# Optimization experiments

Measured on AMD Instinct MI355X. Metric: run time of the kernel, lower is better.

## Reference

```python
import jax, jax.numpy as jnp
import numpy as np

B, T, C, H = 4, 2048, 1024, 16
NEG = -1e9  # masked-fill value (finite to keep grads clean)


def setup_inputs() -> dict:
    key = jax.random.key(0)
    ks = jax.random.split(key, 5)
    s = 1.0 / np.sqrt(C)  # keep logits O(1) like trained linear layers
    return {
        "x": jax.random.normal(ks[0], (B, T, C), dtype=jnp.float32),
        "wq": jax.random.normal(ks[1], (C, C), dtype=jnp.float32) * s,
        "bq": jnp.zeros((C,), dtype=jnp.float32),
        "wk": jax.random.normal(ks[2], (C, C), dtype=jnp.float32) * s,
        "bk": jnp.zeros((C,), dtype=jnp.float32),
        "wv": jax.random.normal(ks[3], (C, C), dtype=jnp.float32) * s,
        "bv": jnp.zeros((C,), dtype=jnp.float32),
        "wo": jax.random.normal(ks[4], (C, C), dtype=jnp.float32) * s,
        "bo": jnp.zeros((C,), dtype=jnp.float32),
    }


def _split_heads(y):
    # [B,T,C] -> [B,H,T,hd]
    b, t, c = y.shape
    return y.reshape(b, t, H, c // H).transpose(0, 2, 1, 3)


def reference(x, wq, bq, wk, bk, wv, bv, wo, bo):
    b, t, c = x.shape
    scale = (c // H) ** (-0.5)
    q = _split_heads(x @ wq.T + bq)  # [B,H,T,hd]
    k = _split_heads(x @ wk.T + bk)
    v = _split_heads(x @ wv.T + bv)
    att = jnp.einsum("bhqd,bhkd->bhqk", q, k) * scale  # [B,H,T,T]
    causal = jnp.tril(jnp.ones((t, t), dtype=bool))
    att = jnp.where(causal[None, None], att, NEG)
    att = jax.nn.softmax(att, axis=-1)  # dropout is identity in eval mode
    y = jnp.einsum("bhqk,bhkd->bhqd", att, v)
    y = y.transpose(0, 2, 1, 3).reshape(b, t, c)
    return y @ wo.T + bo
```

## Files before the change

kernel.cpp:

```cpp
#include <hip/hip_runtime.h>


#define B_ 4
#define T_ 2048
#define C_ 1024
#define H_ 16
#define M_ 8192

typedef unsigned short u16;
typedef __bf16 bf16x8 __attribute__((ext_vector_type(8)));
typedef float f32x4 __attribute__((ext_vector_type(4)));

static __device__ __forceinline__ u16 f2bf(float f) {
  unsigned int u = __float_as_uint(f);
  u += 0x7fffu + ((u >> 16) & 1u);
  return (u16)(u >> 16);
}

static __device__ __forceinline__ void async16(const void* g, void* l) {
  __builtin_amdgcn_global_load_lds(
      (const __attribute__((address_space(1))) unsigned int*)g,
      (__attribute__((address_space(3))) unsigned int*)l, 16, 0, 0);
}

#if __has_builtin(__builtin_amdgcn_exp2f)
#define EXP2F(x) __builtin_amdgcn_exp2f(x)
#else
#define EXP2F(x) exp2f(x)
#endif

static __device__ __forceinline__ f32x4 mfma32(bf16x8 a, bf16x8 b, f32x4 c) {
  return __builtin_amdgcn_mfma_f32_16x16x32_bf16(a, b, c, 0, 0, 0);
}

static __device__ __forceinline__ unsigned int cvtpk(float lo, float hi) {
  unsigned int r;
  asm("v_cvt_pk_bf16_f32 %0, %1, %2" : "=v"(r) : "v"(lo), "v"(hi));
  return r;
}

#define FENCE() asm volatile("" ::: "memory")

__global__ __launch_bounds__(256) void cvt_all(const float* __restrict__ x,
                                               const float* __restrict__ w0,
                                               const float* __restrict__ w1,
                                               const float* __restrict__ w2,
                                               const float* __restrict__ w3,
                                               u16* __restrict__ xb,
                                               u16* __restrict__ wb,
                                               float s0) {
  const int NX = M_ * C_ / 4, NW = C_ * C_ / 4;
  int i = blockIdx.x * 256 + threadIdx.x;
  const float* src;
  u16* dst;
  int idx;
  float s = 1.f;
  if (i < NX) {
    src = x; dst = xb; idx = i;
  } else {
    int j = i - NX;
    int w = j / NW;
    idx = j - w * NW;
    src = (w == 0) ? w0 : (w == 1) ? w1 : (w == 2) ? w2 : w3;
    dst = wb + (size_t)w * C_ * C_;
    if (w == 0) s = s0;
  }
  float4 f = ((const float4*)src)[idx];
  ushort4 o;
  o.x = f2bf(f.x * s); o.y = f2bf(f.y * s); o.z = f2bf(f.z * s); o.w = f2bf(f.w * s);
  ((ushort4*)dst)[idx] = o;
}

__global__ __launch_bounds__(512, 1) void gemm_qkv(const u16* __restrict__ A,
                                                   const u16* __restrict__ W,
                                                   const float* __restrict__ bq,
                                                   const float* __restrict__ bk,
                                                   const float* __restrict__ bv,
                                                   float qscale,
                                                   u16* __restrict__ outqk,
                                                   u16* __restrict__ vtb) {
  __shared__ __align__(16) union {
    u16 buf[3][24576];
    u16 Cu[256 * 136];
    u16 Ct[128 * 272];
  } sm;
  const int tid = threadIdx.x, lane = tid & 63, wave = tid >> 6;
  const int quad = lane >> 4, l16 = lane & 15;
  const int wm = wave >> 1, wn = wave & 1;
  const int bid = blockIdx.x;
  const int xcd = bid & 7, idx = bid >> 3;
  const int cq = idx >> 2;
  const int row0 = (xcd * 4 + (idx & 3)) * 256;
  const int sel = cq >> 3, colw = cq & 7;
  const int col0 = colw * 128;
  const u16* Bt = W + (size_t)sel * C_ * C_;
  const float* bias = sel == 0 ? bq : (sel == 1 ? bk : bv);
  const float bscale = sel == 0 ? qscale : 1.f;

  const u16* aptr[4];
  const u16* bptr[2];
#pragma unroll
  for (int it = 0; it < 4; it++) {
    int c = it * 512 + tid, r = c >> 3, g = (c & 7) ^ (r & 7);
    aptr[it] = A + (size_t)(row0 + r) * C_ + g * 8;
  }
#pragma unroll
  for (int it = 0; it < 2; it++) {
    int c = it * 512 + tid, r = c >> 3, g = (c & 7) ^ (r & 7);
    bptr[it] = Bt + (size_t)(col0 + r) * C_ + g * 8;
  }

  auto STAGE = [&](int t, int pp) {
    const int k0 = t * 64;
    u16* lA = sm.buf[pp];
    u16* lB = sm.buf[pp] + 16384;
#pragma unroll
    for (int it = 0; it < 4; it++)
      async16(aptr[it] + k0, lA + (size_t)(it * 512 + wave * 64) * 8);
#pragma unroll
    for (int it = 0; it < 2; it++)
      async16(bptr[it] + k0, lB + (size_t)(it * 512 + wave * 64) * 8);
  };

  f32x4 zero = {0.f, 0.f, 0.f, 0.f};
  f32x4 acc[4][4];
#pragma unroll
  for (int i = 0; i < 4; i++)
#pragma unroll
    for (int j = 0; j < 4; j++) acc[i][j] = zero;

  STAGE(0, 0);
  STAGE(1, 1);

  int p = 0, p2 = 2;
#pragma unroll 1
  for (int u = 0; u < 16; ++u) {
    FENCE();
    __builtin_amdgcn_s_barrier();
    FENCE();
    if (u < 14) STAGE(u + 2, p2);
    if (u < 14) {
      asm volatile("s_waitcnt vmcnt(12)" ::: "memory");
    } else if (u < 15) {
      asm volatile("s_waitcnt vmcnt(6)" ::: "memory");
    } else {
      asm volatile("s_waitcnt vmcnt(0)" ::: "memory");
    }
    FENCE();
    __builtin_amdgcn_s_barrier();
    FENCE();

    const u16* As = sm.buf[p];
    const u16* Bs = sm.buf[p] + 16384;
    bf16x8 bfr[4][2];
#pragma unroll
    for (int j = 0; j < 4; j++) {
      int rn = wn * 64 + 16 * j + l16;
#pragma unroll
      for (int kk = 0; kk < 2; kk++)
        bfr[j][kk] =
            *(const bf16x8*)(Bs + rn * 64 + (((kk * 4 + quad) ^ (rn & 7)) * 8));
    }
    {
      bf16x8 a2[2][2];
#pragma unroll
      for (int i = 0; i < 2; i++) {
        int rm = wm * 64 + 16 * i + l16;
#pragma unroll
        for (int kk = 0; kk < 2; kk++)
          a2[i][kk] =
              *(const bf16x8*)(As + rm * 64 + (((kk * 4 + quad) ^ (rm & 7)) * 8));
      }
      __builtin_amdgcn_s_setprio(1);
#pragma unroll
      for (int i = 0; i < 2; i++)
#pragma unroll
        for (int j = 0; j < 4; j++) {
          acc[i][j] = mfma32(a2[i][0], bfr[j][0], acc[i][j]);
          acc[i][j] = mfma32(a2[i][1], bfr[j][1], acc[i][j]);
        }
      __builtin_amdgcn_s_setprio(0);
    }
    FENCE();
    __builtin_amdgcn_s_barrier();
    FENCE();
    {
      bf16x8 a2[2][2];
#pragma unroll
      for (int i = 0; i < 2; i++) {
        int rm = wm * 64 + 16 * (i + 2) + l16;
#pragma unroll
        for (int kk = 0; kk < 2; kk++)
          a2[i][kk] =
              *(const bf16x8*)(As + rm * 64 + (((kk * 4 + quad) ^ (rm & 7)) * 8));
      }
      __builtin_amdgcn_s_setprio(1);
#pragma unroll
      for (int i = 0; i < 2; i++)
#pragma unroll
        for (int j = 0; j < 4; j++) {
          acc[i + 2][j] = mfma32(a2[i][0], bfr[j][0], acc[i + 2][j]);
          acc[i + 2][j] = mfma32(a2[i][1], bfr[j][1], acc[i + 2][j]);
        }
      __builtin_amdgcn_s_setprio(0);
    }
    asm volatile("s_waitcnt lgkmcnt(0)" ::: "memory");
    p = (p == 2) ? 0 : p + 1;
    p2 = (p2 == 2) ? 0 : p2 + 1;
  }
  __syncthreads();

  float bj[4];
#pragma unroll
  for (int j = 0; j < 4; j++) bj[j] = bias[col0 + wn * 64 + 16 * j + l16] * bscale;

  if (sel == 2) {
#pragma unroll
    for (int i = 0; i < 4; i++)
#pragma unroll
      for (int j = 0; j < 4; j++) {
        int lc = wn * 64 + 16 * j + l16;
        int rt = wm * 64 + 16 * i + quad * 4;
        union { u16 s[4]; uint2 u; } w;
#pragma unroll
        for (int r = 0; r < 4; r++) w.s[r] = f2bf(acc[i][j][r] + bj[j]);
        *(uint2*)(sm.Ct + (size_t)lc * 272 + rt) = w.u;
      }
    __syncthreads();
    const int bb = row0 >> 11, t0 = row0 & 2047;
#pragma unroll
    for (int c2 = 0; c2 < 8; c2++) {
      int c = c2 * 512 + tid;
      int nr = c >> 5, ch = c & 31;
      bf16x8 v = *(const bf16x8*)(sm.Ct + (size_t)nr * 272 + ch * 8);
      int gn = col0 + nr, d = gn & 63, hh = gn >> 6;
      *(bf16x8*)(vtb + ((size_t)((bb * 16 + hh) * 64 + d)) * T_ + t0 + ch * 8) = v;
    }
  } else {
#pragma unroll
    for (int i = 0; i < 4; i++)
#pragma unroll
      for (int j = 0; j < 4; j++) {
        int lc = wn * 64 + 16 * j + l16;
        int rt = wm * 64 + 16 * i + quad * 4;
#pragma unroll
        for (int r = 0; r < 4; r++)
          sm.Cu[(size_t)(rt + r) * 136 + lc] = f2bf(acc[i][j][r] + bj[j]);
      }
    __syncthreads();
    u16* dst = outqk + (size_t)sel * M_ * C_;
#pragma unroll
    for (int c2 = 0; c2 < 8; c2++) {
      int c = c2 * 512 + tid;
      int rw = c >> 4, ch = c & 15;
      bf16x8 v = *(const bf16x8*)(sm.Cu + (size_t)rw * 136 + ch * 8);
      *(bf16x8*)(dst + (size_t)(row0 + rw) * C_ + col0 + ch * 8) = v;
    }
  }
}

__global__ __launch_bounds__(512, 1) void gemm_o(const u16* __restrict__ A,
                                                 const u16* __restrict__ Bt,
                                                 const float* __restrict__ bias,
                                                 float* __restrict__ outf) {
  __shared__ __align__(16) union {
    u16 buf[3][24576];
    float Cf[256 * 132];
  } sm;
  const int tid = threadIdx.x, lane = tid & 63, wave = tid >> 6;
  const int quad = lane >> 4, l16 = lane & 15;
  const int wm = wave >> 1, wn = wave & 1;
  const int bid = blockIdx.x;
  const int xcd = bid & 7, idx = bid >> 3;
  const int row0 = (xcd * 4 + (idx & 3)) * 256;
  const int col0 = (idx >> 2) * 128;

  const u16* aptr[4];
  const u16* bptr[2];
#pragma unroll
  for (int it = 0; it < 4; it++) {
    int c = it * 512 + tid, r = c >> 3, g = (c & 7) ^ (r & 7);
    aptr[it] = A + (size_t)(row0 + r) * C_ + g * 8;
  }
#pragma unroll
  for (int it = 0; it < 2; it++) {
    int c = it * 512 + tid, r = c >> 3, g = (c & 7) ^ (r & 7);
    bptr[it] = Bt + (size_t)(col0 + r) * C_ + g * 8;
  }

  auto STAGE = [&](int t, int pp) {
    const int k0 = t * 64;
    u16* lA = sm.buf[pp];
    u16* lB = sm.buf[pp] + 16384;
#pragma unroll
    for (int it = 0; it < 4; it++)
      async16(aptr[it] + k0, lA + (size_t)(it * 512 + wave * 64) * 8);
#pragma unroll
    for (int it = 0; it < 2; it++)
      async16(bptr[it] + k0, lB + (size_t)(it * 512 + wave * 64) * 8);
  };

  f32x4 zero = {0.f, 0.f, 0.f, 0.f};
  f32x4 acc[4][4];
#pragma unroll
  for (int i = 0; i < 4; i++)
#pragma unroll
    for (int j = 0; j < 4; j++) acc[i][j] = zero;

  STAGE(0, 0);
  STAGE(1, 1);

  int p = 0, p2 = 2;
#pragma unroll 1
  for (int u = 0; u < 16; ++u) {
    FENCE();
    __builtin_amdgcn_s_barrier();
    FENCE();
    if (u < 14) STAGE(u + 2, p2);
    if (u < 14) {
      asm volatile("s_waitcnt vmcnt(12)" ::: "memory");
    } else if (u < 15) {
      asm volatile("s_waitcnt vmcnt(6)" ::: "memory");
    } else {
      asm volatile("s_waitcnt vmcnt(0)" ::: "memory");
    }
    FENCE();
    __builtin_amdgcn_s_barrier();
    FENCE();

    const u16* As = sm.buf[p];
    const u16* Bs = sm.buf[p] + 16384;
    bf16x8 bfr[4][2];
#pragma unroll
    for (int j = 0; j < 4; j++) {
      int rn = wn * 64 + 16 * j + l16;
#pragma unroll
      for (int kk = 0; kk < 2; kk++)
        bfr[j][kk] =
            *(const bf16x8*)(Bs + rn * 64 + (((kk * 4 + quad) ^ (rn & 7)) * 8));
    }
    {
      bf16x8 a2[2][2];
#pragma unroll
      for (int i = 0; i < 2; i++) {
        int rm = wm * 64 + 16 * i + l16;
#pragma unroll
        for (int kk = 0; kk < 2; kk++)
          a2[i][kk] =
              *(const bf16x8*)(As + rm * 64 + (((kk * 4 + quad) ^ (rm & 7)) * 8));
      }
      __builtin_amdgcn_s_setprio(1);
#pragma unroll
      for (int i = 0; i < 2; i++)
#pragma unroll
        for (int j = 0; j < 4; j++) {
          acc[i][j] = mfma32(a2[i][0], bfr[j][0], acc[i][j]);
          acc[i][j] = mfma32(a2[i][1], bfr[j][1], acc[i][j]);
        }
      __builtin_amdgcn_s_setprio(0);
    }
    FENCE();
    __builtin_amdgcn_s_barrier();
    FENCE();
    {
      bf16x8 a2[2][2];
#pragma unroll
      for (int i = 0; i < 2; i++) {
        int rm = wm * 64 + 16 * (i + 2) + l16;
#pragma unroll
        for (int kk = 0; kk < 2; kk++)
          a2[i][kk] =
              *(const bf16x8*)(As + rm * 64 + (((kk * 4 + quad) ^ (rm & 7)) * 8));
      }
      __builtin_amdgcn_s_setprio(1);
#pragma unroll
      for (int i = 0; i < 2; i++)
#pragma unroll
        for (int j = 0; j < 4; j++) {
          acc[i + 2][j] = mfma32(a2[i][0], bfr[j][0], acc[i + 2][j]);
          acc[i + 2][j] = mfma32(a2[i][1], bfr[j][1], acc[i + 2][j]);
        }
      __builtin_amdgcn_s_setprio(0);
    }
    asm volatile("s_waitcnt lgkmcnt(0)" ::: "memory");
    p = (p == 2) ? 0 : p + 1;
    p2 = (p2 == 2) ? 0 : p2 + 1;
  }
  __syncthreads();

  float bj[4];
#pragma unroll
  for (int j = 0; j < 4; j++) bj[j] = bias[col0 + wn * 64 + 16 * j + l16];

#pragma unroll
  for (int i = 0; i < 4; i++)
#pragma unroll
    for (int j = 0; j < 4; j++) {
      int lc = wn * 64 + 16 * j + l16;
      int rt = wm * 64 + 16 * i + quad * 4;
#pragma unroll
      for (int r = 0; r < 4; r++)
        sm.Cf[(size_t)(rt + r) * 132 + lc] = acc[i][j][r] + bj[j];
    }
  __syncthreads();
#pragma unroll
  for (int c2 = 0; c2 < 16; c2++) {
    int c = c2 * 512 + tid;
    int rw = c >> 5, c4 = c & 31;
    float4 v = *(const float4*)(sm.Cf + (size_t)rw * 132 + c4 * 4);
    *(float4*)(outf + (size_t)(row0 + rw) * C_ + col0 + c4 * 4) = v;
  }
}

__global__ __launch_bounds__(256) void attn(const u16* __restrict__ q,
                                            const u16* __restrict__ k,
                                            const u16* __restrict__ vt,
                                            u16* __restrict__ y) {
  __shared__ __align__(16) u16 Ksm[128 * 64];
  __shared__ __align__(16) u16 Vsm[2][64 * 64];
  const int tid = threadIdx.x, lane = tid & 63, wave = tid >> 6;
  const int quad = lane >> 4, l16 = lane & 15;
  static const int qperm[16] = {15, 14, 11, 10, 12, 13, 8, 9, 3, 2, 7, 6, 0, 1, 4, 5};
  const int bh = blockIdx.x;
  const int qt = qperm[blockIdx.y];
  const int b = bh >> 4, h = bh & 15;

  const int S0 = ((lane & 15) + ((lane >> 4) & 1) * 32) * 4;
  const int S1 = S0 + 64;
  const bool hi32 = (lane & 32) != 0;

  bf16x8 qf[2][2];
#pragma unroll
  for (int m = 0; m < 2; m++) {
    const u16* qp =
        q + (size_t)(b * T_ + qt * 128 + wave * 32 + m * 16 + l16) * C_ + h * 64;
#pragma unroll
    for (int ks = 0; ks < 2; ks++)
      qf[m][ks] = *(const bf16x8*)(qp + ks * 32 + quad * 8);
  }

  f32x4 zero = {0.f, 0.f, 0.f, 0.f};
  f32x4 o[2][4];
  float lps[2] = {0.f, 0.f};
#pragma unroll
  for (int m = 0; m < 2; m++)
#pragma unroll
    for (int dt = 0; dt < 4; dt++) o[m][dt] = zero;

  const u16* kp[4];
  const u16* vp[4];
#pragma unroll
  for (int i = 0; i < 4; i++) {
    int c = i * 256 + tid;
    int r = c >> 3, lc = (c & 7) ^ (r & 7);
    kp[i] = k + (size_t)(b * T_ + r) * C_ + h * 64 + lc * 8;
  }
#pragma unroll
  for (int s = 0; s < 2; s++)
#pragma unroll
    for (int i = 0; i < 2; i++) {
      int c = i * 256 + tid;
      int r = c >> 3, lc = (c & 7) ^ (r & 7);
      vp[s * 2 + i] = vt + (size_t)(bh * 64 + r) * T_ + 64 * s + lc * 8;
    }

  const int qrow = wave * 32 + l16;

#pragma unroll 1
  for (int jt = 0; jt <= qt; ++jt) {
#pragma unroll
    for (int i = 0; i < 4; i++) {
      async16(kp[i], Ksm + (size_t)(i * 256 + wave * 64) * 8);
      kp[i] += (size_t)128 * C_;
    }
#pragma unroll
    for (int s = 0; s < 2; s++)
#pragma unroll
      for (int i = 0; i < 2; i++) {
        async16(vp[s * 2 + i], Vsm[s] + (size_t)(i * 256 + wave * 64) * 8);
        vp[s * 2 + i] += 128;
      }
    __syncthreads();

    const bool diag = (jt == qt);
#pragma unroll
    for (int hh = 0; hh < 2; ++hh) {
      if (diag && (2 * wave + 2 - 4 * hh) <= 0) continue;
      unsigned int pk[2][4][2];
#pragma unroll
      for (int n = 0; n < 4; ++n) {
        int rk = hh * 64 + n * 16 + l16;
        bf16x8 kf0 = *(const bf16x8*)(Ksm + rk * 64 + ((quad ^ (rk & 7)) * 8));
        bf16x8 kf1 = *(const bf16x8*)(Ksm + rk * 64 + (((4 + quad) ^ (rk & 7)) * 8));
#pragma unroll
        for (int m = 0; m < 2; ++m) {
          int nlim = diag ? (2 * wave + m + 1 - 4 * hh) : 4;
          float e[4];
          if (n < nlim) {
            f32x4 s = mfma32(kf0, qf[m][0], zero);
            s = mfma32(kf1, qf[m][1], s);
#pragma unroll
            for (int r = 0; r < 4; r++) e[r] = EXP2F(s[r]);
            if (diag) {
              int rmax = qrow + m * 16 - hh * 64 - n * 16 - quad * 4;
#pragma unroll
              for (int r = 0; r < 4; r++)
                if (r > rmax) e[r] = 0.f;
            }
            lps[m] += (e[0] + e[1]) + (e[2] + e[3]);
          } else {
#pragma unroll
            for (int r = 0; r < 4; r++) e[r] = 0.f;
          }
          pk[m][n][0] = cvtpk(e[0], e[1]);
          pk[m][n][1] = cvtpk(e[2], e[3]);
        }
      }
      bf16x8 pa[2][2];
#pragma unroll
      for (int m = 0; m < 2; ++m)
#pragma unroll
        for (int ks = 0; ks < 2; ++ks) {
          union { unsigned int u[4]; bf16x8 v; } uu;
#pragma unroll
          for (int c = 0; c < 2; ++c) {
            int x = (int)pk[m][2 * ks][c];
            int yv = (int)pk[m][2 * ks + 1][c];
            int bx0 = __builtin_amdgcn_ds_bpermute(S0, x);
            int by0 = __builtin_amdgcn_ds_bpermute(S0, yv);
            int bx1 = __builtin_amdgcn_ds_bpermute(S1, x);
            int by1 = __builtin_amdgcn_ds_bpermute(S1, yv);
            uu.u[c] = (unsigned int)(hi32 ? by0 : bx0);
            uu.u[2 + c] = (unsigned int)(hi32 ? by1 : bx1);
          }
          pa[m][ks] = uu.v;
        }
#pragma unroll
      for (int dt = 0; dt < 4; ++dt) {
        int rv = dt * 16 + l16;
        bf16x8 vf0 = *(const bf16x8*)(Vsm[hh] + rv * 64 + ((quad ^ (rv & 7)) * 8));
        bf16x8 vf1 = *(const bf16x8*)(Vsm[hh] + rv * 64 + (((4 + quad) ^ (rv & 7)) * 8));
#pragma unroll
        for (int m = 0; m < 2; m++) {
          o[m][dt] = mfma32(pa[m][0], vf0, o[m][dt]);
          o[m][dt] = mfma32(pa[m][1], vf1, o[m][dt]);
        }
      }
    }
    __syncthreads();
  }

  float linv[2];
#pragma unroll
  for (int m = 0; m < 2; m++) {
    float v = lps[m];
    v += __shfl_xor(v, 16);
    v += __shfl_xor(v, 32);
    linv[m] = 1.f / v;
  }

#pragma unroll
  for (int m = 0; m < 2; m++)
#pragma unroll
    for (int r = 0; r < 4; r++) {
      float il = __shfl(linv[m], quad * 4 + r);
      int grow = b * T_ + qt * 128 + wave * 32 + m * 16 + quad * 4 + r;
#pragma unroll
      for (int dt = 0; dt < 4; dt++)
        y[(size_t)grow * C_ + h * 64 + dt * 16 + l16] = f2bf(o[m][dt][r] * il);
    }
}

extern "C" void kernel_launch(void* const* d_in, const int* in_sizes, int n_in,
                              void* d_out, int out_size, void* d_ws, size_t ws_size,
                              hipStream_t stream) {
  const float* x  = (const float*)d_in[0];
  const float* wq = (const float*)d_in[1];
  const float* bq = (const float*)d_in[2];
  const float* wk = (const float*)d_in[3];
  const float* bk = (const float*)d_in[4];
  const float* wv = (const float*)d_in[5];
  const float* bv = (const float*)d_in[6];
  const float* wo = (const float*)d_in[7];
  const float* bo = (const float*)d_in[8];
  float* out = (float*)d_out;

  const float QSCALE = 0.125f * 1.4426950408889634f;

  u16* xb  = (u16*)d_ws;
  u16* wqb = xb  + (size_t)M_ * C_;
  u16* wob = wqb + 3 * (size_t)C_ * C_;
  u16* qb  = wob + (size_t)C_ * C_;
  u16* kb  = qb  + (size_t)M_ * C_;
  u16* vtb = kb  + (size_t)M_ * C_;
  u16* yb  = xb;

  const int NCVT = (M_ * C_ + 4 * C_ * C_) / 4 / 256;
  cvt_all<<<NCVT, 256, 0, stream>>>(x, wq, wk, wv, wo, xb, wqb, QSCALE);

  gemm_qkv<<<768, 512, 0, stream>>>(xb, wqb, bq, bk, bv, QSCALE, qb, vtb);

  attn<<<dim3(B_ * H_, 16), 256, 0, stream>>>(qb, kb, vtb, yb);

  gemm_o<<<256, 512, 0, stream>>>(yb, wob, bo, out);
}
```

Before: 251.5 us.

## Pair complementary causal query tiles per block and register-prefetch K/V tiles

Each attention block now handles query tile qtA and its mirror 15-qtA, so the causal work per block is even and each K/V tile loaded serves both tiles. The asynchronous global-to-LDS loads are replaced by register prefetching of the next K/V tile, which is written into LDS between two barriers. The grid drops to 512 blocks and register use rises, with two accumulator sets and the prefetch registers, which can lower occupancy.

```diff
diff --git a/kernel.cpp b/kernel.cpp
--- a/kernel.cpp
+++ b/kernel.cpp
@@ -420,32 +420,36 @@
   __shared__ __align__(16) u16 Vsm[2][64 * 64];
   const int tid = threadIdx.x, lane = tid & 63, wave = tid >> 6;
   const int quad = lane >> 4, l16 = lane & 15;
-  static const int qperm[16] = {15, 14, 11, 10, 12, 13, 8, 9, 3, 2, 7, 6, 0, 1, 4, 5};
   const int bh = blockIdx.x;
-  const int qt = qperm[blockIdx.y];
+  const int qtA = blockIdx.y;
+  const int qtB = 15 - qtA;
   const int b = bh >> 4, h = bh & 15;
 
   const int S0 = ((lane & 15) + ((lane >> 4) & 1) * 32) * 4;
   const int S1 = S0 + 64;
   const bool hi32 = (lane & 32) != 0;
 
-  bf16x8 qf[2][2];
+  bf16x8 qfA[2][2], qfB[2][2];
 #pragma unroll
   for (int m = 0; m < 2; m++) {
-    const u16* qp =
-        q + (size_t)(b * T_ + qt * 128 + wave * 32 + m * 16 + l16) * C_ + h * 64;
-#pragma unroll
-    for (int ks = 0; ks < 2; ks++)
-      qf[m][ks] = *(const bf16x8*)(qp + ks * 32 + quad * 8);
+    const u16* qpA =
+        q + (size_t)(b * T_ + qtA * 128 + wave * 32 + m * 16 + l16) * C_ + h * 64;
+    const u16* qpB =
+        q + (size_t)(b * T_ + qtB * 128 + wave * 32 + m * 16 + l16) * C_ + h * 64;
+#pragma unroll
+    for (int ks = 0; ks < 2; ks++) {
+      qfA[m][ks] = *(const bf16x8*)(qpA + ks * 32 + quad * 8);
+      qfB[m][ks] = *(const bf16x8*)(qpB + ks * 32 + quad * 8);
+    }
   }
 
   f32x4 zero = {0.f, 0.f, 0.f, 0.f};
-  f32x4 o[2][4];
-  float lps[2] = {0.f, 0.f};
+  f32x4 oA[2][4], oB[2][4];
+  float lpsA[2] = {0.f, 0.f}, lpsB[2] = {0.f, 0.f};
 #pragma unroll
   for (int m = 0; m < 2; m++)
 #pragma unroll
-    for (int dt = 0; dt < 4; dt++) o[m][dt] = zero;
+    for (int dt = 0; dt < 4; dt++) { oA[m][dt] = zero; oB[m][dt] = zero; }
 
   const u16* kp[4];
   const u16* vp[4];
@@ -464,25 +468,22 @@
       vp[s * 2 + i] = vt + (size_t)(bh * 64 + r) * T_ + 64 * s + lc * 8;
     }
 
+  uint4 kreg[4], vreg[4];
+  auto loadKV = [&](int jt) {
+    const size_t koff = (size_t)jt * 128 * C_;
+    const int voff = jt * 128;
+#pragma unroll
+    for (int i = 0; i < 4; i++)
+      kreg[i] = *(const uint4*)(kp[i] + koff);
+#pragma unroll
+    for (int i = 0; i < 4; i++)
+      vreg[i] = *(const uint4*)(vp[i] + voff);
+  };
+
   const int qrow = wave * 32 + l16;
 
-#pragma unroll 1
-  for (int jt = 0; jt <= qt; ++jt) {
-#pragma unroll
-    for (int i = 0; i < 4; i++) {
-      async16(kp[i], Ksm + (size_t)(i * 256 + wave * 64) * 8);
-      kp[i] += (size_t)128 * C_;
-    }
-#pragma unroll
-    for (int s = 0; s < 2; s++)
-#pragma unroll
-      for (int i = 0; i < 2; i++) {
-        async16(vp[s * 2 + i], Vsm[s] + (size_t)(i * 256 + wave * 64) * 8);
-        vp[s * 2 + i] += 128;
-      }
-    __syncthreads();
-
-    const bool diag = (jt == qt);
+  auto tileCompute = [&](const bf16x8 (&qf)[2][2], f32x4 (&o)[2][4],
+                         float (&lps)[2], const bool diag) {
 #pragma unroll
     for (int hh = 0; hh < 2; ++hh) {
       if (diag && (2 * wave + 2 - 4 * hh) <= 0) continue;
@@ -547,27 +548,60 @@
         }
       }
     }
-    __syncthreads();
-  }
-
-  float linv[2];
+  };
+
+  loadKV(0);
+
+#pragma unroll 1
+  for (int jt = 0; jt <= qtB; ++jt) {
+    FENCE();
+    __builtin_amdgcn_s_barrier();
+    FENCE();
+#pragma unroll
+    for (int i = 0; i < 4; i++)
+      *(uint4*)(Ksm + (size_t)(i * 256 + tid) * 8) = kreg[i];
+#pragma unroll
+    for (int s = 0; s < 2; s++)
+#pragma unroll
+      for (int i = 0; i < 2; i++)
+        *(uint4*)(Vsm[s] + (size_t)(i * 256 + tid) * 8) = vreg[s * 2 + i];
+    if (jt < qtB) loadKV(jt + 1);
+    asm volatile("s_waitcnt lgkmcnt(0)" ::: "memory");
+    FENCE();
+    __builtin_amdgcn_s_barrier();
+    FENCE();
+
+    if (jt <= qtA) tileCompute(qfA, oA, lpsA, jt == qtA);
+    tileCompute(qfB, oB, lpsB, jt == qtB);
+    asm volatile("s_waitcnt lgkmcnt(0)" ::: "memory");
+  }
+
+  float linvA[2], linvB[2];
 #pragma unroll
   for (int m = 0; m < 2; m++) {
-    float v = lps[m];
+    float v = lpsA[m];
     v += __shfl_xor(v, 16);
     v += __shfl_xor(v, 32);
-    linv[m] = 1.f / v;
+    linvA[m] = 1.f / v;
+    float w = lpsB[m];
+    w += __shfl_xor(w, 16);
+    w += __shfl_xor(w, 32);
+    linvB[m] = 1.f / w;
   }
 
 #pragma unroll
   for (int m = 0; m < 2; m++)
 #pragma unroll
     for (int r = 0; r < 4; r++) {
-      float il = __shfl(linv[m], quad * 4 + r);
-      int grow = b * T_ + qt * 128 + wave * 32 + m * 16 + quad * 4 + r;
-#pragma unroll
-      for (int dt = 0; dt < 4; dt++)
-        y[(size_t)grow * C_ + h * 64 + dt * 16 + l16] = f2bf(o[m][dt][r] * il);
+      float ilA = __shfl(linvA[m], quad * 4 + r);
+      float ilB = __shfl(linvB[m], quad * 4 + r);
+      int growA = b * T_ + qtA * 128 + wave * 32 + m * 16 + quad * 4 + r;
+      int growB = b * T_ + qtB * 128 + wave * 32 + m * 16 + quad * 4 + r;
+#pragma unroll
+      for (int dt = 0; dt < 4; dt++) {
+        y[(size_t)growA * C_ + h * 64 + dt * 16 + l16] = f2bf(oA[m][dt][r] * ilA);
+        y[(size_t)growB * C_ + h * 64 + dt * 16 + l16] = f2bf(oB[m][dt][r] * ilB);
+      }
     }
 }
 
@@ -600,7 +634,7 @@
 
   gemm_qkv<<<768, 512, 0, stream>>>(xb, wqb, bq, bk, bv, QSCALE, qb, vtb);
 
-  attn<<<dim3(B_ * H_, 16), 256, 0, stream>>>(qb, kb, vtb, yb);
+  attn<<<dim3(B_ * H_, 8), 256, 0, stream>>>(qb, kb, vtb, yb);
 
   gemm_o<<<256, 512, 0, stream>>>(yb, wob, bo, out);
 }
```

After: 289.9 us. 1.15x slower.

## Split attention into single-wave blocks reading K/V directly from global memory

Applied to the files above, without the earlier changes.

The attention kernel moves from 256-thread blocks, which stage K and V tiles in LDS with async loads and barriers, to 64-thread single-wave blocks. Each block handles 32 query rows and loads its K and V fragments straight from global memory, relying on cache. Block ids are remapped so that blocks sharing a (batch, head) land on the same XCD, which should improve L2 reuse. This removes LDS use and __syncthreads, and smaller blocks should help occupancy and load balance. In exchange, four waves now fetch the same K/V data separately, which raises global/L2 traffic, and the loads are no longer asynchronous or shared.

```diff
diff --git a/kernel.cpp b/kernel.cpp
--- a/kernel.cpp
+++ b/kernel.cpp
@@ -412,17 +412,20 @@
   }
 }
 
-__global__ __launch_bounds__(256) void attn(const u16* __restrict__ q,
-                                            const u16* __restrict__ k,
-                                            const u16* __restrict__ vt,
-                                            u16* __restrict__ y) {
-  __shared__ __align__(16) u16 Ksm[128 * 64];
-  __shared__ __align__(16) u16 Vsm[2][64 * 64];
-  const int tid = threadIdx.x, lane = tid & 63, wave = tid >> 6;
+__global__ __launch_bounds__(64) void attn(const u16* __restrict__ q,
+                                           const u16* __restrict__ k,
+                                           const u16* __restrict__ vt,
+                                           u16* __restrict__ y) {
+  const int lane = threadIdx.x;
   const int quad = lane >> 4, l16 = lane & 15;
   static const int qperm[16] = {15, 14, 11, 10, 12, 13, 8, 9, 3, 2, 7, 6, 0, 1, 4, 5};
-  const int bh = blockIdx.x;
-  const int qt = qperm[blockIdx.y];
+  const int bid = blockIdx.x;
+  const int xcd = bid & 7, idx = bid >> 3;
+  const int lin = xcd * 512 + idx;
+  const int bh = lin >> 6;
+  const int rem = lin & 63;
+  const int qt = qperm[rem >> 2];
+  const int wv = rem & 3;
   const int b = bh >> 4, h = bh & 15;
 
   const int S0 = ((lane & 15) + ((lane >> 4) & 1) * 32) * 4;
@@ -433,7 +436,7 @@
 #pragma unroll
   for (int m = 0; m < 2; m++) {
     const u16* qp =
-        q + (size_t)(b * T_ + qt * 128 + wave * 32 + m * 16 + l16) * C_ + h * 64;
+        q + (size_t)(b * T_ + qt * 128 + wv * 32 + m * 16 + l16) * C_ + h * 64;
 #pragma unroll
     for (int ks = 0; ks < 2; ks++)
       qf[m][ks] = *(const bf16x8*)(qp + ks * 32 + quad * 8);
@@ -447,54 +450,28 @@
 #pragma unroll
     for (int dt = 0; dt < 4; dt++) o[m][dt] = zero;
 
-  const u16* kp[4];
-  const u16* vp[4];
-#pragma unroll
-  for (int i = 0; i < 4; i++) {
-    int c = i * 256 + tid;
-    int r = c >> 3, lc = (c & 7) ^ (r & 7);
-    kp[i] = k + (size_t)(b * T_ + r) * C_ + h * 64 + lc * 8;
-  }
-#pragma unroll
-  for (int s = 0; s < 2; s++)
-#pragma unroll
-    for (int i = 0; i < 2; i++) {
-      int c = i * 256 + tid;
-      int r = c >> 3, lc = (c & 7) ^ (r & 7);
-      vp[s * 2 + i] = vt + (size_t)(bh * 64 + r) * T_ + 64 * s + lc * 8;
-    }
-
-  const int qrow = wave * 32 + l16;
+  const u16* kb = k + (size_t)(b * T_) * C_ + h * 64;
+  const u16* vb = vt + (size_t)(bh * 64) * T_;
+  const int qrow = wv * 32 + l16;
 
 #pragma unroll 1
   for (int jt = 0; jt <= qt; ++jt) {
-#pragma unroll
-    for (int i = 0; i < 4; i++) {
-      async16(kp[i], Ksm + (size_t)(i * 256 + wave * 64) * 8);
-      kp[i] += (size_t)128 * C_;
-    }
-#pragma unroll
-    for (int s = 0; s < 2; s++)
-#pragma unroll
-      for (int i = 0; i < 2; i++) {
-        async16(vp[s * 2 + i], Vsm[s] + (size_t)(i * 256 + wave * 64) * 8);
-        vp[s * 2 + i] += 128;
-      }
-    __syncthreads();
-
+    const u16* kt = kb + (size_t)(jt * 128) * C_;
+    const u16* vtp = vb + jt * 128;
     const bool diag = (jt == qt);
 #pragma unroll
     for (int hh = 0; hh < 2; ++hh) {
-      if (diag && (2 * wave + 2 - 4 * hh) <= 0) continue;
+      if (diag && (2 * wv + 2 - 4 * hh) <= 0) continue;
       unsigned int pk[2][4][2];
 #pragma unroll
       for (int n = 0; n < 4; ++n) {
         int rk = hh * 64 + n * 16 + l16;
-        bf16x8 kf0 = *(const bf16x8*)(Ksm + rk * 64 + ((quad ^ (rk & 7)) * 8));
-        bf16x8 kf1 = *(const bf16x8*)(Ksm + rk * 64 + (((4 + quad) ^ (rk & 7)) * 8));
+        const u16* krow = kt + (size_t)rk * C_;
+        bf16x8 kf0 = *(const bf16x8*)(krow + quad * 8);
+        bf16x8 kf1 = *(const bf16x8*)(krow + 32 + quad * 8);
 #pragma unroll
         for (int m = 0; m < 2; ++m) {
-          int nlim = diag ? (2 * wave + m + 1 - 4 * hh) : 4;
+          int nlim = diag ? (2 * wv + m + 1 - 4 * hh) : 4;
           float e[4];
           if (n < nlim) {
             f32x4 s = mfma32(kf0, qf[m][0], zero);
@@ -538,8 +515,9 @@
 #pragma unroll
       for (int dt = 0; dt < 4; ++dt) {
         int rv = dt * 16 + l16;
-        bf16x8 vf0 = *(const bf16x8*)(Vsm[hh] + rv * 64 + ((quad ^ (rv & 7)) * 8));
-        bf16x8 vf1 = *(const bf16x8*)(Vsm[hh] + rv * 64 + (((4 + quad) ^ (rv & 7)) * 8));
+        const u16* vrow = vtp + (size_t)rv * T_ + hh * 64;
+        bf16x8 vf0 = *(const bf16x8*)(vrow + quad * 8);
+        bf16x8 vf1 = *(const bf16x8*)(vrow + 32 + quad * 8);
 #pragma unroll
         for (int m = 0; m < 2; m++) {
           o[m][dt] = mfma32(pa[m][0], vf0, o[m][dt]);
@@ -547,7 +525,6 @@
         }
       }
     }
-    __syncthreads();
   }
 
   float linv[2];
@@ -564,7 +541,7 @@
 #pragma unroll
     for (int r = 0; r < 4; r++) {
       float il = __shfl(linv[m], quad * 4 + r);
-      int grow = b * T_ + qt * 128 + wave * 32 + m * 16 + quad * 4 + r;
+      int grow = b * T_ + qt * 128 + wv * 32 + m * 16 + quad * 4 + r;
 #pragma unroll
       for (int dt = 0; dt < 4; dt++)
         y[(size_t)grow * C_ + h * 64 + dt * 16 + l16] = f2bf(o[m][dt][r] * il);
@@ -600,7 +577,7 @@
 
   gemm_qkv<<<768, 512, 0, stream>>>(xb, wqb, bq, bk, bv, QSCALE, qb, vtb);
 
-  attn<<<dim3(B_ * H_, 16), 256, 0, stream>>>(qb, kb, vtb, yb);
+  attn<<<4096, 64, 0, stream>>>(qb, kb, vtb, yb);
 
   gemm_o<<<256, 512, 0, stream>>>(yb, wob, bo, out);
 }
```

Result: slower. 359.5 us (+42.9%).
